# Kernel tuning notes

Measured on AMD Instinct MI355X. Metric: run time of the kernel, lower is better.

## Reference

```python
import jax, jax.numpy as jnp
import numpy as np

DIM = 1024
HEADS = 16
HEAD_DIM = DIM // HEADS
SCALE = HEAD_DIM ** -0.5


def setup_inputs() -> dict:
    key = jax.random.key(0)
    k1, k2, k3, k4 = jax.random.split(key, 4)
    x = jax.random.normal(k1, (8, 1024, DIM), dtype=jnp.float32)
    # nn.Linear weight is [out, in]; init ~ small values
    W_qkv = jax.random.normal(k2, (3 * DIM, DIM), dtype=jnp.float32) * 0.02
    W_proj = jax.random.normal(k3, (DIM, DIM), dtype=jnp.float32) * 0.02
    b_proj = jax.random.normal(k4, (DIM,), dtype=jnp.float32) * 0.02
    return {"x": x, "W_qkv": W_qkv, "W_proj": W_proj, "b_proj": b_proj}


def reference(x, W_qkv, W_proj, b_proj):
    b, n, _ = x.shape
    h, d = HEADS, HEAD_DIM
    qkv = x @ W_qkv.T  # [b, n, 3*dim]
    # rearrange 'b n (qkv h d) -> qkv b h n d'
    qkv = qkv.reshape(b, n, 3, h, d).transpose(2, 0, 3, 1, 4)
    q, k, v = qkv[0], qkv[1], qkv[2]  # each [b, h, n, d]
    dots = jnp.einsum('bhid,bhjd->bhij', q, k) * SCALE
    attn = jax.nn.softmax(dots, axis=-1)
    out = jnp.einsum('bhij,bhjd->bhid', attn, v)
    out = out.transpose(0, 2, 1, 3).reshape(b, n, h * d)  # b n (h d)
    return out @ W_proj.T + b_proj
```

## Files before the change

kernel.cpp:

```cpp
#include <hip/hip_runtime.h>
#include <math.h>

#define DIM   1024
#define HEADS 16
#define HDIM  64
#define SEQ   1024
#define BATCH 8
#define QSCALE 0.1803368801111204f
#define LDH   72
#define ABM   128

typedef __attribute__((ext_vector_type(8)))  short          short8_t;
typedef __attribute__((ext_vector_type(8)))  unsigned short ushort8_t;
typedef __attribute__((ext_vector_type(4)))  unsigned short ushort4_t;
typedef __attribute__((ext_vector_type(4)))  float          floatx4;
typedef __attribute__((ext_vector_type(16))) float          floatx16;

__device__ __forceinline__ unsigned short f2bf(float f) {
    unsigned u = __float_as_uint(f);
    u += 0x7fffu + ((u >> 16) & 1u);
    return (unsigned short)(u >> 16);
}
__device__ __forceinline__ unsigned rnd_bf(float f) {
    unsigned u = __float_as_uint(f);
    return u + 0x7fffu + ((u >> 16) & 1u);
}
__device__ __forceinline__ float fast_exp2(float x) {
#if __has_builtin(__builtin_amdgcn_exp2f)
    return __builtin_amdgcn_exp2f(x);
#else
    return exp2f(x);
#endif
}
__device__ __forceinline__ void glds16(const unsigned short* g, unsigned short* l) {
    __builtin_amdgcn_global_load_lds(
        (const __attribute__((address_space(1))) void*)g,
        (__attribute__((address_space(3))) void*)l, 16, 0, 0);
}

__global__ __launch_bounds__(256) void cvt_bf16_all(const float* __restrict__ x,
                                                    const float* __restrict__ wqkv,
                                                    const float* __restrict__ wproj,
                                                    unsigned short* __restrict__ x_o,
                                                    unsigned short* __restrict__ wqkv_o,
                                                    unsigned short* __restrict__ wproj_o) {
    const int N8_X = BATCH * SEQ * DIM / 8;
    const int N8_WQ = 3 * DIM * DIM / 8;
    const int N8_WP = DIM * DIM / 8;
    int i = blockIdx.x * 256 + threadIdx.x;
    const float* in;
    unsigned short* out;
    if (i < N8_X)               { in = x;     out = x_o; }
    else if (i < N8_X + N8_WQ)  { i -= N8_X;  in = wqkv; out = wqkv_o; }
    else                        { i -= N8_X + N8_WQ;
                                  if (i >= N8_WP) return;
                                  in = wproj; out = wproj_o; }
    const float4* p = (const float4*)in + (size_t)i * 2;
    float4 a = p[0], b = p[1];
    ushort8_t u;
    u[0] = f2bf(a.x); u[1] = f2bf(a.y); u[2] = f2bf(a.z); u[3] = f2bf(a.w);
    u[4] = f2bf(b.x); u[5] = f2bf(b.y); u[6] = f2bf(b.z); u[7] = f2bf(b.w);
    ((ushort8_t*)out)[i] = u;
}

template<int MODE>
__global__ __launch_bounds__(256) void gemm_nt_mfma(const unsigned short* __restrict__ A,
                                                    const unsigned short* __restrict__ B,
                                                    const float* __restrict__ bias,
                                                    void* __restrict__ Cout,
                                                    unsigned short* __restrict__ vt,
                                                    int M, int N, int K) {
    __shared__ __align__(16) unsigned short As[128 * 64];
    __shared__ __align__(16) unsigned short Bs[128 * 64];

    const int tid  = threadIdx.x;
    const int lane = tid & 63;
    const int wave = tid >> 6;
    const int wm = (wave >> 1) * 64;
    const int wn = (wave & 1) * 64;
    const size_t brow = (size_t)blockIdx.x * 128;
    const size_t bcol = (size_t)blockIdx.y * 128;

    const int srow   = lane >> 3;
    const int schunk = (lane & 7) ^ srow;
    const unsigned short* gA = A + (brow + wave * 8 + srow) * (size_t)K + schunk * 8;
    const unsigned short* gB = B + (bcol + wave * 8 + srow) * (size_t)K + schunk * 8;
    unsigned short* lA = &As[wave * 512 + lane * 8];
    unsigned short* lB = &Bs[wave * 512 + lane * 8];

    floatx16 acc[2][2];
    #pragma unroll
    for (int i = 0; i < 2; i++)
        #pragma unroll
        for (int j = 0; j < 2; j++)
            #pragma unroll
            for (int r = 0; r < 16; r++) acc[i][j][r] = 0.f;

    const int c32  = lane & 31;
    const int half = lane >> 5;
    const int xr   = c32 & 7;

    for (int k0 = 0; k0 < K; k0 += 64) {
        __syncthreads();
        #pragma unroll
        for (int r = 0; r < 4; r++) {
            glds16(gA + (size_t)r * 32 * K + k0, lA + r * 2048);
            glds16(gB + (size_t)r * 32 * K + k0, lB + r * 2048);
        }
        __syncthreads();

        #pragma unroll
        for (int s = 0; s < 4; s++) {
            const int ch = ((s * 2 + half) ^ xr) * 8;
            short8_t a0 = *(const short8_t*)&As[(wm + c32) * 64 + ch];
            short8_t a1 = *(const short8_t*)&As[(wm + 32 + c32) * 64 + ch];
            short8_t b0 = *(const short8_t*)&Bs[(wn + c32) * 64 + ch];
            short8_t b1 = *(const short8_t*)&Bs[(wn + 32 + c32) * 64 + ch];
            acc[0][0] = __builtin_amdgcn_mfma_f32_32x32x16_bf16(a0, b0, acc[0][0], 0, 0, 0);
            acc[0][1] = __builtin_amdgcn_mfma_f32_32x32x16_bf16(a0, b1, acc[0][1], 0, 0, 0);
            acc[1][0] = __builtin_amdgcn_mfma_f32_32x32x16_bf16(a1, b0, acc[1][0], 0, 0, 0);
            acc[1][1] = __builtin_amdgcn_mfma_f32_32x32x16_bf16(a1, b1, acc[1][1], 0, 0, 0);
        }
    }

    if (MODE == 0) {
        #pragma unroll
        for (int mi = 0; mi < 2; mi++)
            #pragma unroll
            for (int ni = 0; ni < 2; ni++) {
                const size_t col = bcol + wn + ni * 32 + c32;
                const float bv = bias[col];
                #pragma unroll
                for (int r = 0; r < 16; r++) {
                    const size_t row = brow + wm + mi * 32 + (r & 3) + 8 * (r >> 2) + 4 * half;
                    ((float*)Cout)[row * N + col] = acc[mi][ni][r] + bv;
                }
            }
    } else {
        if (bcol < 2048) {
            const float sc = (bcol < 1024) ? QSCALE : 1.0f;
            unsigned short* qk = (unsigned short*)Cout;
            #pragma unroll
            for (int mi = 0; mi < 2; mi++)
                #pragma unroll
                for (int ni = 0; ni < 2; ni++) {
                    const size_t col = bcol + wn + ni * 32 + c32;
                    #pragma unroll
                    for (int r = 0; r < 16; r++) {
                        const size_t row = brow + wm + mi * 32 + (r & 3) + 8 * (r >> 2) + 4 * half;
                        qk[row * 2048 + col] = f2bf(acc[mi][ni][r] * sc);
                    }
                }
        } else {
            #pragma unroll
            for (int mi = 0; mi < 2; mi++)
                #pragma unroll
                for (int ni = 0; ni < 2; ni++) {
                    const int dall = (int)(bcol + wn + ni * 32 + c32) - 2048;
                    const int h = dall >> 6, d = dall & 63;
                    #pragma unroll
                    for (int rg = 0; rg < 4; rg++) {
                        const size_t row0 = brow + wm + mi * 32 + rg * 8 + 4 * half;
                        const size_t bb = row0 >> 10;
                        const int n0 = (int)(row0 & 1023);
                        ushort4_t o;
                        #pragma unroll
                        for (int q = 0; q < 4; q++) o[q] = f2bf(acc[mi][ni][rg * 4 + q]);
                        *(ushort4_t*)&vt[(((size_t)bb * HEADS + h) * HDIM + d) * SEQ + n0] = o;
                    }
                }
        }
    }
}

__global__ __launch_bounds__(256) void attn_mfma(const unsigned short* __restrict__ qk,
                                                 const unsigned short* __restrict__ vt,
                                                 unsigned short* __restrict__ aout) {
    const int bh = blockIdx.x;
    const int qt = blockIdx.y;
    const int h  = bh & 15;
    const int b  = bh >> 4;
    const int tid  = threadIdx.x;
    const int lane = tid & 63;
    const int wave = tid >> 6;
    const int g = lane >> 4;
    const int c = lane & 15;

    __shared__ __align__(16) unsigned short Qs[ABM * LDH];
    __shared__ __align__(16) unsigned short Ks[2][64 * 64];
    __shared__ __align__(16) unsigned short Vs[2][64 * 64];
    __shared__ float scr[4][2][16];

    const int sr = tid >> 2;
    const int sq = tid & 3;
    const int sx = sr & 7;
    const unsigned short* ksrc0 =
        qk + ((size_t)(b * SEQ + sr)) * 2048 + DIM + h * HDIM + sq * 16;
    const unsigned short* vsrc0 =
        vt + (((size_t)(b * HEADS + h)) * HDIM + sr) * SEQ + sq * 16;
    const int kvo0 = sr * 64 + (((sq * 2)     ^ sx) * 8);
    const int kvo1 = sr * 64 + (((sq * 2 + 1) ^ sx) * 8);

    ushort8_t ck0 = *(const ushort8_t*)ksrc0;
    ushort8_t ck1 = *(const ushort8_t*)(ksrc0 + 8);
    ushort8_t cv0 = *(const ushort8_t*)vsrc0;
    ushort8_t cv1 = *(const ushort8_t*)(vsrc0 + 8);

    {
        const int r  = tid >> 1;
        const int c0 = (tid & 1) * 32;
        const unsigned short* src =
            qk + ((size_t)(b * SEQ + qt * ABM + r)) * 2048 + h * HDIM + c0;
        unsigned short* dst = &Qs[r * LDH + c0];
        *(ushort8_t*)(dst)      = *(const ushort8_t*)(src);
        *(ushort8_t*)(dst + 8)  = *(const ushort8_t*)(src + 8);
        *(ushort8_t*)(dst + 16) = *(const ushort8_t*)(src + 16);
        *(ushort8_t*)(dst + 24) = *(const ushort8_t*)(src + 24);
    }
    __syncthreads();

    short8_t bq[2][2];
    #pragma unroll
    for (int f = 0; f < 2; f++)
        #pragma unroll
        for (int kc = 0; kc < 2; kc++)
            bq[f][kc] = *(const short8_t*)&Qs[(f * 64 + wave * 16 + c) * LDH + g * 8 + kc * 32];

    floatx4 O[2][4];
    #pragma unroll
    for (int f = 0; f < 2; f++)
        #pragma unroll
        for (int i = 0; i < 4; i++) O[f][i] = (floatx4){0.f, 0.f, 0.f, 0.f};
    float lsum[2] = {0.f, 0.f};

    const int fro0 = ((0 * 4 + g) ^ (c & 7)) * 8;
    const int fro1 = ((1 * 4 + g) ^ (c & 7)) * 8;

    for (int kt = 0; kt < SEQ / 64; kt++) {
        const int cur = kt & 1;
        *(ushort8_t*)&Ks[cur][kvo0] = ck0;
        *(ushort8_t*)&Ks[cur][kvo1] = ck1;
        *(ushort8_t*)&Vs[cur][kvo0] = cv0;
        *(ushort8_t*)&Vs[cur][kvo1] = cv1;
        __syncthreads();
        if (kt + 1 < SEQ / 64) {
            const unsigned short* ks = ksrc0 + (size_t)(kt + 1) * 64 * 2048;
            const unsigned short* vs = vsrc0 + (kt + 1) * 64;
            ck0 = *(const ushort8_t*)ks;
            ck1 = *(const ushort8_t*)(ks + 8);
            cv0 = *(const ushort8_t*)vs;
            cv1 = *(const ushort8_t*)(vs + 8);
        }

        short8_t ak[4][2];
        #pragma unroll
        for (int nt = 0; nt < 4; nt++) {
            ak[nt][0] = *(const short8_t*)&Ks[cur][(nt * 16 + c) * 64 + fro0];
            ak[nt][1] = *(const short8_t*)&Ks[cur][(nt * 16 + c) * 64 + fro1];
        }

        floatx4 S[2][4];
        #pragma unroll
        for (int f = 0; f < 2; f++)
            #pragma unroll
            for (int nt = 0; nt < 4; nt++) S[f][nt] = (floatx4){0.f, 0.f, 0.f, 0.f};
        #pragma unroll
        for (int f = 0; f < 2; f++)
            #pragma unroll
            for (int nt = 0; nt < 4; nt++)
                #pragma unroll
                for (int kc = 0; kc < 2; kc++)
                    S[f][nt] = __builtin_amdgcn_mfma_f32_16x16x32_bf16(
                        ak[nt][kc], bq[f][kc], S[f][nt], 0, 0, 0);

        #pragma unroll
        for (int f = 0; f < 2; f++)
            #pragma unroll
            for (int nt = 0; nt < 4; nt++) {
                const float p0 = fast_exp2(S[f][nt][0]);
                const float p1 = fast_exp2(S[f][nt][1]);
                const float p2 = fast_exp2(S[f][nt][2]);
                const float p3 = fast_exp2(S[f][nt][3]);
                lsum[f] += (p0 + p1) + (p2 + p3);
                const unsigned r01 = __builtin_amdgcn_perm(rnd_bf(p1), rnd_bf(p0), 0x07060302);
                const unsigned r23 = __builtin_amdgcn_perm(rnd_bf(p3), rnd_bf(p2), 0x07060302);
                *(uint2*)&Qs[(f * 64 + wave * 16 + c) * LDH + nt * 16 + g * 4] =
                    make_uint2(r01, r23);
            }

        short8_t bv[4][2];
        #pragma unroll
        for (int dnt = 0; dnt < 4; dnt++) {
            bv[dnt][0] = *(const short8_t*)&Vs[cur][(dnt * 16 + c) * 64 + fro0];
            bv[dnt][1] = *(const short8_t*)&Vs[cur][(dnt * 16 + c) * 64 + fro1];
        }

        #pragma unroll
        for (int f = 0; f < 2; f++) {
            short8_t ap[2];
            #pragma unroll
            for (int kc = 0; kc < 2; kc++)
                ap[kc] = *(const short8_t*)&Qs[(f * 64 + wave * 16 + c) * LDH + g * 8 + kc * 32];
            #pragma unroll
            for (int dnt = 0; dnt < 4; dnt++)
                #pragma unroll
                for (int kc = 0; kc < 2; kc++)
                    O[f][dnt] = __builtin_amdgcn_mfma_f32_16x16x32_bf16(
                        ap[kc], bv[dnt][kc], O[f][dnt], 0, 0, 0);
        }
    }

    #pragma unroll
    for (int f = 0; f < 2; f++) {
        float s = lsum[f];
        s += __shfl_xor(s, 16);
        s += __shfl_xor(s, 32);
        if (g == 0) scr[wave][f][c] = 1.0f / s;
    }
    __builtin_amdgcn_s_waitcnt(0);

    #pragma unroll
    for (int f = 0; f < 2; f++) {
        const float4 inv4 = *(const float4*)&scr[wave][f][g * 4];
        #pragma unroll
        for (int r = 0; r < 4; r++) {
            const float invl = ((const float*)&inv4)[r];
            const size_t row = (size_t)b * SEQ + qt * ABM + f * 64 + wave * 16 + g * 4 + r;
            #pragma unroll
            for (int dnt = 0; dnt < 4; dnt++)
                aout[row * DIM + h * HDIM + dnt * 16 + c] = f2bf(O[f][dnt][r] * invl);
        }
    }
}

extern "C" void kernel_launch(void* const* d_in, const int* in_sizes, int n_in,
                              void* d_out, int out_size, void* d_ws, size_t ws_size,
                              hipStream_t stream) {
    const float* x      = (const float*)d_in[0];
    const float* W_qkv  = (const float*)d_in[1];
    const float* W_proj = (const float*)d_in[2];
    const float* b_proj = (const float*)d_in[3];
    float* out = (float*)d_out;

    const int M = BATCH * SEQ;

    unsigned short* ws       = (unsigned short*)d_ws;
    unsigned short* x_bf     = ws;
    unsigned short* wqkv_bf  = x_bf + (size_t)M * DIM;
    unsigned short* wproj_bf = wqkv_bf + (size_t)3 * DIM * DIM;
    unsigned short* qk_bf    = wproj_bf + (size_t)DIM * DIM;
    unsigned short* vt_bf    = qk_bf + (size_t)M * 2048;
    unsigned short* aout_bf  = vt_bf + (size_t)BATCH * HEADS * HDIM * SEQ;

    {
        const int n8 = (M * DIM + 3 * DIM * DIM + DIM * DIM) / 8;
        cvt_bf16_all<<<(n8 + 255) / 256, 256, 0, stream>>>(
            x, W_qkv, W_proj, x_bf, wqkv_bf, wproj_bf);
    }

    gemm_nt_mfma<2><<<dim3(M / 128, 3 * DIM / 128), 256, 0, stream>>>(
        x_bf, wqkv_bf, nullptr, qk_bf, vt_bf, M, 3 * DIM, DIM);

    attn_mfma<<<dim3(BATCH * HEADS, SEQ / ABM), 256, 0, stream>>>(qk_bf, vt_bf, aout_bf);

    gemm_nt_mfma<0><<<dim3(M / 128, DIM / 128), 256, 0, stream>>>(
        aout_bf, wproj_bf, b_proj, out, nullptr, M, DIM, DIM);
}
```

Baseline: 234.2 us.

## Switch attention kernel from 16x16x32 to 32x32x16 bf16 MFMA tiles

Rewrites the attention inner loop so each wave owns 32 contiguous query rows and uses 32x32x16 MFMA instructions for both QK^T and PV instead of 16x16x32. Fragment loads, the P write-back into shared memory, row-sum reduction and the output epilogue are remapped to the 32x32 accumulator layout. The intent is fewer MFMA issues and fewer LDS fragment loads per unit of work, giving higher matrix-core throughput. It risks new LDS bank conflicts under the changed swizzle/access pattern and different register pressure from the floatx16 accumulators.

```diff
diff --git a/kernel.cpp b/kernel.cpp
--- a/kernel.cpp
+++ b/kernel.cpp
@@ -183,13 +183,13 @@
     const int tid  = threadIdx.x;
     const int lane = tid & 63;
     const int wave = tid >> 6;
-    const int g = lane >> 4;
-    const int c = lane & 15;
+    const int c32  = lane & 31;
+    const int half = lane >> 5;
 
     __shared__ __align__(16) unsigned short Qs[ABM * LDH];
     __shared__ __align__(16) unsigned short Ks[2][64 * 64];
     __shared__ __align__(16) unsigned short Vs[2][64 * 64];
-    __shared__ float scr[4][2][16];
+    __shared__ float scr[4][32];
 
     const int sr = tid >> 2;
     const int sq = tid & 3;
@@ -219,22 +219,19 @@
     }
     __syncthreads();
 
-    short8_t bq[2][2];
+    short8_t bq[4];
     #pragma unroll
-    for (int f = 0; f < 2; f++)
-        #pragma unroll
-        for (int kc = 0; kc < 2; kc++)
-            bq[f][kc] = *(const short8_t*)&Qs[(f * 64 + wave * 16 + c) * LDH + g * 8 + kc * 32];
-
-    floatx4 O[2][4];
+    for (int s = 0; s < 4; s++)
+        bq[s] = *(const short8_t*)&Qs[(wave * 32 + c32) * LDH + s * 16 + half * 8];
+
+    floatx16 O[2];
     #pragma unroll
-    for (int f = 0; f < 2; f++)
-        #pragma unroll
-        for (int i = 0; i < 4; i++) O[f][i] = (floatx4){0.f, 0.f, 0.f, 0.f};
-    float lsum[2] = {0.f, 0.f};
-
-    const int fro0 = ((0 * 4 + g) ^ (c & 7)) * 8;
-    const int fro1 = ((1 * 4 + g) ^ (c & 7)) * 8;
+    for (int dt = 0; dt < 2; dt++)
+        #pragma unroll
+        for (int r = 0; r < 16; r++) O[dt][r] = 0.f;
+    float lsum = 0.f;
+
+    const int fxr = c32 & 7;
 
     for (int kt = 0; kt < SEQ / 64; kt++) {
         const int cur = kt & 1;
@@ -252,83 +249,63 @@
             cv1 = *(const ushort8_t*)(vs + 8);
         }
 
-        short8_t ak[4][2];
-        #pragma unroll
-        for (int nt = 0; nt < 4; nt++) {
-            ak[nt][0] = *(const short8_t*)&Ks[cur][(nt * 16 + c) * 64 + fro0];
-            ak[nt][1] = *(const short8_t*)&Ks[cur][(nt * 16 + c) * 64 + fro1];
-        }
-
-        floatx4 S[2][4];
-        #pragma unroll
-        for (int f = 0; f < 2; f++)
-            #pragma unroll
-            for (int nt = 0; nt < 4; nt++) S[f][nt] = (floatx4){0.f, 0.f, 0.f, 0.f};
-        #pragma unroll
-        for (int f = 0; f < 2; f++)
-            #pragma unroll
-            for (int nt = 0; nt < 4; nt++)
-                #pragma unroll
-                for (int kc = 0; kc < 2; kc++)
-                    S[f][nt] = __builtin_amdgcn_mfma_f32_16x16x32_bf16(
-                        ak[nt][kc], bq[f][kc], S[f][nt], 0, 0, 0);
-
-        #pragma unroll
-        for (int f = 0; f < 2; f++)
-            #pragma unroll
-            for (int nt = 0; nt < 4; nt++) {
-                const float p0 = fast_exp2(S[f][nt][0]);
-                const float p1 = fast_exp2(S[f][nt][1]);
-                const float p2 = fast_exp2(S[f][nt][2]);
-                const float p3 = fast_exp2(S[f][nt][3]);
-                lsum[f] += (p0 + p1) + (p2 + p3);
+        floatx16 S[2];
+        #pragma unroll
+        for (int t = 0; t < 2; t++)
+            #pragma unroll
+            for (int r = 0; r < 16; r++) S[t][r] = 0.f;
+        #pragma unroll
+        for (int t = 0; t < 2; t++)
+            #pragma unroll
+            for (int s = 0; s < 4; s++) {
+                const int slot = ((s * 2 + half) ^ fxr) * 8;
+                short8_t ak = *(const short8_t*)&Ks[cur][(t * 32 + c32) * 64 + slot];
+                S[t] = __builtin_amdgcn_mfma_f32_32x32x16_bf16(ak, bq[s], S[t], 0, 0, 0);
+            }
+
+        #pragma unroll
+        for (int t = 0; t < 2; t++)
+            #pragma unroll
+            for (int rg = 0; rg < 4; rg++) {
+                const float p0 = fast_exp2(S[t][rg * 4 + 0]);
+                const float p1 = fast_exp2(S[t][rg * 4 + 1]);
+                const float p2 = fast_exp2(S[t][rg * 4 + 2]);
+                const float p3 = fast_exp2(S[t][rg * 4 + 3]);
+                lsum += (p0 + p1) + (p2 + p3);
                 const unsigned r01 = __builtin_amdgcn_perm(rnd_bf(p1), rnd_bf(p0), 0x07060302);
                 const unsigned r23 = __builtin_amdgcn_perm(rnd_bf(p3), rnd_bf(p2), 0x07060302);
-                *(uint2*)&Qs[(f * 64 + wave * 16 + c) * LDH + nt * 16 + g * 4] =
+                *(uint2*)&Qs[(wave * 32 + c32) * LDH + t * 32 + rg * 8 + 4 * half] =
                     make_uint2(r01, r23);
             }
 
-        short8_t bv[4][2];
-        #pragma unroll
-        for (int dnt = 0; dnt < 4; dnt++) {
-            bv[dnt][0] = *(const short8_t*)&Vs[cur][(dnt * 16 + c) * 64 + fro0];
-            bv[dnt][1] = *(const short8_t*)&Vs[cur][(dnt * 16 + c) * 64 + fro1];
-        }
-
-        #pragma unroll
-        for (int f = 0; f < 2; f++) {
-            short8_t ap[2];
-            #pragma unroll
-            for (int kc = 0; kc < 2; kc++)
-                ap[kc] = *(const short8_t*)&Qs[(f * 64 + wave * 16 + c) * LDH + g * 8 + kc * 32];
-            #pragma unroll
-            for (int dnt = 0; dnt < 4; dnt++)
-                #pragma unroll
-                for (int kc = 0; kc < 2; kc++)
-                    O[f][dnt] = __builtin_amdgcn_mfma_f32_16x16x32_bf16(
-                        ap[kc], bv[dnt][kc], O[f][dnt], 0, 0, 0);
-        }
-    }
+        short8_t ap[4];
+        #pragma unroll
+        for (int s = 0; s < 4; s++)
+            ap[s] = *(const short8_t*)&Qs[(wave * 32 + c32) * LDH + s * 16 + half * 8];
+        #pragma unroll
+        for (int dt = 0; dt < 2; dt++)
+            #pragma unroll
+            for (int s = 0; s < 4; s++) {
+                const int slot = ((s * 2 + half) ^ fxr) * 8;
+                short8_t bv = *(const short8_t*)&Vs[cur][(dt * 32 + c32) * 64 + slot];
+                O[dt] = __builtin_amdgcn_mfma_f32_32x32x16_bf16(ap[s], bv, O[dt], 0, 0, 0);
+            }
+    }
+
+    lsum += __shfl_xor(lsum, 32);
+    if (half == 0) scr[wave][c32] = 1.0f / lsum;
+    __builtin_amdgcn_s_waitcnt(0);
 
     #pragma unroll
-    for (int f = 0; f < 2; f++) {
-        float s = lsum[f];
-        s += __shfl_xor(s, 16);
-        s += __shfl_xor(s, 32);
-        if (g == 0) scr[wave][f][c] = 1.0f / s;
-    }
-    __builtin_amdgcn_s_waitcnt(0);
-
-    #pragma unroll
-    for (int f = 0; f < 2; f++) {
-        const float4 inv4 = *(const float4*)&scr[wave][f][g * 4];
-        #pragma unroll
-        for (int r = 0; r < 4; r++) {
-            const float invl = ((const float*)&inv4)[r];
-            const size_t row = (size_t)b * SEQ + qt * ABM + f * 64 + wave * 16 + g * 4 + r;
-            #pragma unroll
-            for (int dnt = 0; dnt < 4; dnt++)
-                aout[row * DIM + h * HDIM + dnt * 16 + c] = f2bf(O[f][dnt][r] * invl);
+    for (int rg = 0; rg < 4; rg++) {
+        const float4 inv4 = *(const float4*)&scr[wave][rg * 8 + 4 * half];
+        #pragma unroll
+        for (int q = 0; q < 4; q++) {
+            const float invl = ((const float*)&inv4)[q];
+            const size_t row = (size_t)b * SEQ + qt * ABM + wave * 32 + rg * 8 + 4 * half + q;
+            #pragma unroll
+            for (int dt = 0; dt < 2; dt++)
+                aout[row * DIM + h * HDIM + dt * 32 + c32] = f2bf(O[dt][rg * 4 + q] * invl);
         }
     }
 }
```

New measurement: 231.0 us. Within noise of the previous version (-1.3%).
